# Kernel tuning notes

Hardware: AMD Instinct MI355X
Metric: run time of the kernel (lower is better)

## Reference

```python
import jax, jax.numpy as jnp
import numpy as np

N, D, IN_DIM, H, L = 20000, 32, 3, 64, 3


def _lstm_agg(h_nodes, nbr_sorted, W_ih, W_hh, b_ih, b_hh):
    """Batched LSTM over each node's (sorted) neighbor sequence; returns final hidden state h_T."""
    n = h_nodes.shape[0]
    hidden = W_hh.shape[1]

    def step(carry, idx):
        h, c = carry
        x = h_nodes[idx]                                     # [N, in_d] irregular gather
        gates = x @ W_ih.T + h @ W_hh.T + b_ih + b_hh        # [N, 4H], torch gate order i,f,g,o
        i_g, f_g, g_g, o_g = jnp.split(gates, 4, axis=-1)
        c = jax.nn.sigmoid(f_g) * c + jax.nn.sigmoid(i_g) * jnp.tanh(g_g)
        h = jax.nn.sigmoid(o_g) * jnp.tanh(c)
        return (h, c), None

    init = (jnp.zeros((n, hidden), h_nodes.dtype), jnp.zeros((n, hidden), h_nodes.dtype))
    (h_T, _), _ = jax.lax.scan(step, init, nbr_sorted.T)      # scan over D neighbor slots
    return h_T


def _layer(h, nbr_sorted, W_ih, W_hh, b_ih, b_hh, Wl, bl):
    agg = _lstm_agg(h, nbr_sorted, W_ih, W_hh, b_ih, b_hh)    # [N, H]
    comb = jnp.concatenate([h, agg], axis=-1)                 # [N, in_d + H]
    return jax.nn.relu(comb @ Wl.T + bl)


def _forward(node_features, nbr, params, W_out, b_out):
    nbr_sorted = jnp.sort(nbr, axis=1)   # permutation-invariant ordering (Eq. 9)
    h = node_features
    for p in params:
        h = _layer(h, nbr_sorted, *p)
    return (h @ W_out.T + b_out).squeeze(-1)   # [N] per-node log-likelihood scores


def setup_inputs():
    key = jax.random.key(0)
    ks = jax.random.split(key, 40)
    inp = {}
    inp["node_features"] = jax.random.normal(ks[0], (N, IN_DIM), jnp.float32)
    inp["nbr"] = jax.random.randint(ks[1], (N, D), 0, N, jnp.int32)
    k = 2
    s = 1.0 / np.sqrt(H)
    for l in range(L):
        in_d = IN_DIM if l == 0 else H
        inp[f"W_ih{l}"] = (jax.random.normal(ks[k], (4 * H, in_d)) * (1.0 / np.sqrt(in_d))).astype(jnp.float32); k += 1
        inp[f"W_hh{l}"] = (jax.random.normal(ks[k], (4 * H, H)) * s).astype(jnp.float32); k += 1
        inp[f"b_ih{l}"] = (jax.random.normal(ks[k], (4 * H,)) * s).astype(jnp.float32); k += 1
        inp[f"b_hh{l}"] = (jax.random.normal(ks[k], (4 * H,)) * s).astype(jnp.float32); k += 1
        inp[f"Wl{l}"] = (jax.random.normal(ks[k], (H, in_d + H)) * (1.0 / np.sqrt(in_d + H))).astype(jnp.float32); k += 1
        inp[f"bl{l}"] = (jax.random.normal(ks[k], (H,)) * s).astype(jnp.float32); k += 1
    inp["W_out"] = (jax.random.normal(ks[k], (1, H)) * s).astype(jnp.float32); k += 1
    inp["b_out"] = jnp.zeros((1,), jnp.float32)
    return inp


def reference(node_features, nbr, W_ih0, W_hh0, b_ih0, b_hh0, Wl0, bl0, W_ih1, W_hh1, b_ih1, b_hh1, Wl1, bl1, W_ih2, W_hh2, b_ih2, b_hh2, Wl2, bl2, W_out, b_out):
    params = [
        (W_ih0, W_hh0, b_ih0, b_hh0, Wl0, bl0),
        (W_ih1, W_hh1, b_ih1, b_hh1, Wl1, bl1),
        (W_ih2, W_hh2, b_ih2, b_hh2, Wl2, bl2),
    ]
    return _forward(node_features, nbr, params, W_out, b_out)
```

## Files before the change

### kernel.cpp

```cpp
#include <hip/hip_runtime.h>
#include <hip/hip_bf16.h>

#define NN 20000
#define NG 1250
#define LOG2E 1.44269504088896f
#define TWOLOG2E 2.88539008177793f

typedef __attribute__((ext_vector_type(8))) short short8;
typedef __attribute__((ext_vector_type(4))) float floatx4;

__device__ __forceinline__ floatx4 MF(short8 a, short8 b, floatx4 c) {
    return __builtin_amdgcn_mfma_f32_16x16x32_bf16(a, b, c, 0, 0, 0);
}
__device__ __forceinline__ float ex2(float x) { return __builtin_amdgcn_exp2f(x); }
__device__ __forceinline__ float rcp(float x) { return __builtin_amdgcn_rcpf(x); }
__device__ __forceinline__ unsigned short bf16r(float x) {
    return __builtin_bit_cast(unsigned short, __float2bfloat16(x));
}
__device__ __forceinline__ void lds_barrier() {
    asm volatile("s_waitcnt lgkmcnt(0)\n\ts_barrier" ::: "memory");
}
__device__ __forceinline__ int rowswz(int L) {
    return L ^ (((L >> 4) & 1) << 1) ^ ((L >> 3) & 1);
}

__global__ void sort_nbrs_kernel(const int* __restrict__ nbr, int* __restrict__ nbrT) {
    int n = blockIdx.x * blockDim.x + threadIdx.x;
    if (n >= NN) return;
    int v[32];
    const int4* src = (const int4*)(nbr + n * 32);
    #pragma unroll
    for (int i = 0; i < 8; i++) {
        int4 t = src[i];
        v[4*i] = t.x; v[4*i+1] = t.y; v[4*i+2] = t.z; v[4*i+3] = t.w;
    }
    #pragma unroll
    for (int k = 2; k <= 32; k <<= 1)
        #pragma unroll
        for (int j = k >> 1; j > 0; j >>= 1)
            #pragma unroll
            for (int i = 0; i < 32; i++) {
                int ixj = i ^ j;
                if (ixj > i) {
                    bool up = (i & k) == 0;
                    int a = v[i], b = v[ixj];
                    bool sw = up ? (a > b) : (a < b);
                    if (sw) { v[i] = b; v[ixj] = a; }
                }
            }
    int g = n >> 4, m = n & 15;
    int base = g * 512 + m;
    #pragma unroll
    for (int t = 0; t < 32; t++) nbrT[base + t * 16] = v[t];
}

#define PREP_TOT (49152 + 49152 + 12288 + 12288 + 768 + 640000)
__global__ void prep_kernel(const float* __restrict__ x,
    const float* __restrict__ Wih0, const float* __restrict__ Whh0,
    const float* __restrict__ bih0, const float* __restrict__ bhh0, const float* __restrict__ Wl0,
    const float* __restrict__ Wih1, const float* __restrict__ Whh1,
    const float* __restrict__ bih1, const float* __restrict__ bhh1, const float* __restrict__ Wl1,
    const float* __restrict__ Wih2, const float* __restrict__ Whh2,
    const float* __restrict__ bih2, const float* __restrict__ bhh2, const float* __restrict__ Wl2,
    unsigned short* __restrict__ Wih_p, unsigned short* __restrict__ Whh_p,
    unsigned short* __restrict__ Wlx_p, unsigned short* __restrict__ Wlh_p,
    float* __restrict__ bsum, unsigned short* __restrict__ x32)
{
    for (int i = blockIdx.x * 256 + threadIdx.x; i < PREP_TOT; i += gridDim.x * 256) {
        int j = i;
        if (j < 49152) {
            int l = j >> 14, e = j & 16383;
            if (l == 0) {
                if (e < 8192) {
                    int col = e >> 5, k = e & 31;
                    float sc = (col >= 128 && col < 192) ? TWOLOG2E : LOG2E;
                    float v = (k < 3) ? Wih0[col*3 + k] * sc : 0.f;
                    Wih_p[e] = bf16r(v);
                }
            } else {
                int col = e >> 6, k = e & 63;
                const float* W = (l == 1) ? Wih1 : Wih2;
                float sc = (col >= 128 && col < 192) ? TWOLOG2E : LOG2E;
                Wih_p[l*16384 + e] = bf16r(W[col*64 + k] * sc);
            }
            continue;
        }
        j -= 49152;
        if (j < 49152) {
            int l = j >> 14, e = j & 16383;
            int col = e >> 6, k = e & 63;
            const float* W = (l == 0) ? Whh0 : ((l == 1) ? Whh1 : Whh2);
            float sc = (col >= 128 && col < 192) ? TWOLOG2E : LOG2E;
            Whh_p[l*16384 + e] = bf16r(W[col*64 + k] * sc);
            continue;
        }
        j -= 49152;
        if (j < 12288) {
            int l = j >> 12, e = j & 4095;
            if (l == 0) {
                if (e < 2048) {
                    int col = e >> 5, k = e & 31;
                    float v = (k < 3) ? Wl0[col*67 + k] : 0.f;
                    Wlx_p[e] = bf16r(v);
                }
            } else {
                int col = e >> 6, k = e & 63;
                const float* W = (l == 1) ? Wl1 : Wl2;
                Wlx_p[l*4096 + e] = bf16r(W[col*128 + k]);
            }
            continue;
        }
        j -= 12288;
        if (j < 12288) {
            int l = j >> 12, e = j & 4095;
            int col = e >> 6, k = e & 63;
            float v = (l == 0) ? Wl0[col*67 + 3 + k]
                               : ((l == 1) ? Wl1 : Wl2)[col*128 + 64 + k];
            Wlh_p[l*4096 + e] = bf16r(v);
            continue;
        }
        j -= 12288;
        if (j < 768) {
            int l = j >> 8, col = j & 255;
            const float* bi = (l == 0) ? bih0 : ((l == 1) ? bih1 : bih2);
            const float* bh = (l == 0) ? bhh0 : ((l == 1) ? bhh1 : bhh2);
            float sc = (col >= 128 && col < 192) ? TWOLOG2E : LOG2E;
            bsum[l*256 + col] = (bi[col] + bh[col]) * sc;
            continue;
        }
        j -= 768;
        {
            int n = j >> 5, k = j & 31;
            x32[j] = bf16r((k < 3) ? x[n*3 + k] : 0.f);
        }
    }
}

template<int XKC, int LASTL>
__global__ __launch_bounds__(256, 3)
void lstm_mfma_kernel(const unsigned short* __restrict__ xsrc,
                      const int* __restrict__ nbrT,
                      const unsigned short* __restrict__ Wih,
                      const unsigned short* __restrict__ Whh,
                      const float* __restrict__ bsum,
                      const unsigned short* __restrict__ Wlx,
                      const unsigned short* __restrict__ Wlh,
                      const float* __restrict__ bl,
                      const float* __restrict__ W_out,
                      const float* __restrict__ b_out,
                      void* __restrict__ hout)
{
    __shared__ unsigned short sA[2][1024];
    __shared__ float sRed[64];

    const int w    = threadIdx.x >> 6;
    const int lane = threadIdx.x & 63;
    const int q    = lane >> 4;
    const int c    = lane & 15;
    const int XS   = XKC * 32;

    const int g = blockIdx.x;
    const int node0 = g * 16;
    const int* nbg = nbrT + g * 512;

    short8 fWih[4][XKC];
    short8 fWhh[4][2];
    float  biasv[4];
    #pragma unroll
    for (int t4 = 0; t4 < 4; t4++) {
        int col = 64*t4 + 16*w + c;
        biasv[t4] = bsum[col];
        #pragma unroll
        for (int kc = 0; kc < XKC; kc++)
            fWih[t4][kc] = *(const short8*)(Wih + col*XS + kc*32 + q*8);
        #pragma unroll
        for (int kc = 0; kc < 2; kc++)
            fWhh[t4][kc] = *(const short8*)(Whh + col*64 + kc*32 + q*8);
    }

    float cst[4] = {0.f, 0.f, 0.f, 0.f};
    short8 hA[2] = {};

    int idx_cur = nbg[c];
    int idx_nxt = nbg[16 + c];
    short8 xg[XKC];
    #pragma unroll
    for (int kc = 0; kc < XKC; kc++)
        xg[kc] = *(const short8*)(xsrc + (long)idx_cur * XS + kc*32 + q*8);

    #pragma unroll 1
    for (int t = 0; t < 32; t++) {
        floatx4 acc[4];
        #pragma unroll
        for (int t4 = 0; t4 < 4; t4++) {
            floatx4 a; a[0] = biasv[t4]; a[1] = biasv[t4]; a[2] = biasv[t4]; a[3] = biasv[t4];
            acc[t4] = a;
        }
        if (t > 0) {
            #pragma unroll
            for (int t4 = 0; t4 < 4; t4++) {
                acc[t4] = MF(hA[0], fWhh[t4][0], acc[t4]);
                acc[t4] = MF(hA[1], fWhh[t4][1], acc[t4]);
            }
        }
        #pragma unroll
        for (int t4 = 0; t4 < 4; t4++)
            #pragma unroll
            for (int kc = 0; kc < XKC; kc++)
                acc[t4] = MF(xg[kc], fWih[t4][kc], acc[t4]);

        if (t < 31) {
            #pragma unroll
            for (int kc = 0; kc < XKC; kc++)
                xg[kc] = *(const short8*)(xsrc + (long)idx_nxt * XS + kc*32 + q*8);
            int tn = (t + 2 < 32) ? t + 2 : 31;
            idx_nxt = nbg[tn*16 + c];
        }

        unsigned short* sAb = sA[t & 1];
        const int u = 16*w + c;
        #pragma unroll
        for (int r = 0; r < 4; r++) {
            float gi = acc[0][r], gf = acc[1][r], gg = acc[2][r], go = acc[3][r];
            float ei = ex2(-gi);
            float ef = ex2(-gf);
            float eo = ex2(-go);
            float eg = ex2(-__builtin_fabsf(gg));
            float iG = __builtin_copysignf(1.f - eg, gg) * rcp((1.f + ei) * (1.f + eg));
            float cm = fmaf(cst[r], rcp(1.f + ef), iG);
            cst[r] = cm;
            float ec = ex2(-TWOLOG2E * __builtin_fabsf(cm));
            float h  = __builtin_copysignf(1.f - ec, cm) * rcp((1.f + eo) * (1.f + ec));
            int row = (4*q + r) + 16*(u >> 3);
            sAb[rowswz(row)*8 + (u & 7)] = bf16r(h);
        }
        lds_barrier();
        hA[0] = *(const short8*)(sA[t & 1] + rowswz(lane)*8);
        hA[1] = *(const short8*)(sA[t & 1] + 512 + rowswz(lane)*8);
    }

    const int col = 16*w + c;
    short8 fx[XKC], fh[2];
    float blv = bl[col];
    #pragma unroll
    for (int kc = 0; kc < XKC; kc++)
        fx[kc] = *(const short8*)(Wlx + col*XS + kc*32 + q*8);
    fh[0] = *(const short8*)(Wlh + col*64 + q*8);
    fh[1] = *(const short8*)(Wlh + col*64 + 32 + q*8);
    short8 hin[XKC];
    #pragma unroll
    for (int kc = 0; kc < XKC; kc++)
        hin[kc] = *(const short8*)(xsrc + (long)(node0 + c) * XS + kc*32 + q*8);

    floatx4 a; a[0] = blv; a[1] = blv; a[2] = blv; a[3] = blv;
    #pragma unroll
    for (int kc = 0; kc < XKC; kc++) a = MF(hin[kc], fx[kc], a);
    a = MF(hA[0], fh[0], a);
    a = MF(hA[1], fh[1], a);

    if (!LASTL) {
        #pragma unroll
        for (int r = 0; r < 4; r++)
            ((unsigned short*)hout)[(node0 + 4*q + r) * 64 + col] = bf16r(fmaxf(a[r], 0.f));
    } else {
        float wo = W_out[col];
        float p[4];
        #pragma unroll
        for (int r = 0; r < 4; r++) p[r] = fmaxf(a[r], 0.f) * wo;
        #pragma unroll
        for (int d = 1; d < 16; d <<= 1) {
            #pragma unroll
            for (int r = 0; r < 4; r++) p[r] += __shfl_xor(p[r], d);
        }
        if (c == 0) {
            #pragma unroll
            for (int r = 0; r < 4; r++) sRed[w*16 + 4*q + r] = p[r];
        }
        lds_barrier();
        if (w == 0 && lane < 16)
            ((float*)hout)[node0 + lane] =
                sRed[lane] + sRed[16 + lane] + sRed[32 + lane] + sRed[48 + lane] + b_out[0];
    }
}

extern "C" void kernel_launch(void* const* d_in, const int* in_sizes, int n_in,
                              void* d_out, int out_size, void* d_ws, size_t ws_size,
                              hipStream_t stream) {
    (void)in_sizes; (void)n_in; (void)out_size; (void)ws_size;
    const float* node_features = (const float*)d_in[0];
    const int*   nbr           = (const int*)d_in[1];
    const float* Wih[3] = {(const float*)d_in[2],  (const float*)d_in[8],  (const float*)d_in[14]};
    const float* Whh[3] = {(const float*)d_in[3],  (const float*)d_in[9],  (const float*)d_in[15]};
    const float* bih[3] = {(const float*)d_in[4],  (const float*)d_in[10], (const float*)d_in[16]};
    const float* bhh[3] = {(const float*)d_in[5],  (const float*)d_in[11], (const float*)d_in[17]};
    const float* Wl[3]  = {(const float*)d_in[6],  (const float*)d_in[12], (const float*)d_in[18]};
    const float* bl[3]  = {(const float*)d_in[7],  (const float*)d_in[13], (const float*)d_in[19]};
    const float* W_out  = (const float*)d_in[20];
    const float* b_out  = (const float*)d_in[21];

    char* ws = (char*)d_ws;
    int*            nbrT  = (int*)ws;
    unsigned short* x32   = (unsigned short*)(ws + 2560000);
    unsigned short* hb1   = (unsigned short*)(ws + 3840000);
    unsigned short* hb2   = (unsigned short*)(ws + 6400000);
    unsigned short* Wih_p = (unsigned short*)(ws + 8960000);
    unsigned short* Whh_p = (unsigned short*)(ws + 9058304);
    unsigned short* Wlx_p = (unsigned short*)(ws + 9156608);
    unsigned short* Wlh_p = (unsigned short*)(ws + 9181184);
    float*          bsum  = (float*)(ws + 9205760);

    prep_kernel<<<1024, 256, 0, stream>>>(node_features,
        Wih[0], Whh[0], bih[0], bhh[0], Wl[0],
        Wih[1], Whh[1], bih[1], bhh[1], Wl[1],
        Wih[2], Whh[2], bih[2], bhh[2], Wl[2],
        Wih_p, Whh_p, Wlx_p, Wlh_p, bsum, x32);
    sort_nbrs_kernel<<<(NN + 255) / 256, 256, 0, stream>>>(nbr, nbrT);

    lstm_mfma_kernel<1, 0><<<NG, 256, 0, stream>>>(x32, nbrT,
        Wih_p,         Whh_p,         bsum,       Wlx_p,        Wlh_p,        bl[0],
        nullptr, nullptr, hb1);
    lstm_mfma_kernel<2, 0><<<NG, 256, 0, stream>>>(hb1, nbrT,
        Wih_p + 16384, Whh_p + 16384, bsum + 256, Wlx_p + 4096, Wlh_p + 4096, bl[1],
        nullptr, nullptr, hb2);
    lstm_mfma_kernel<2, 1><<<NG, 256, 0, stream>>>(hb2, nbrT,
        Wih_p + 32768, Whh_p + 32768, bsum + 512, Wlx_p + 8192, Wlh_p + 8192, bl[2],
        W_out, b_out, (float*)d_out);
}
```

Before: 297.1 us.

## Interleave two node groups per block and precompute input gates a step ahead

Each block now processes 32 nodes as two independent 16-node LSTM chains, interleaving their MFMAs and cell math so the serial recurrence latency of one chain is hidden by the other. The input-to-hidden MFMAs for the next step are issued right after the cell update, ahead of the barrier, and the gather prefetch runs one step further ahead. The second half of the W_ih fragments moves to LDS to save registers, and the neighbor sort is folded into the prep kernel to remove a launch. In exchange, register pressure is higher and the grid shrinks to 625 blocks, which lowers occupancy and wave-level parallelism.

```diff
diff --git a/kernel.cpp b/kernel.cpp
--- a/kernel.cpp
+++ b/kernel.cpp
@@ -2,7 +2,7 @@
 #include <hip/hip_bf16.h>
 
 #define NN 20000
-#define NG 1250
+#define NGB 625
 #define LOG2E 1.44269504088896f
 #define TWOLOG2E 2.88539008177793f
 
@@ -24,38 +24,27 @@
     return L ^ (((L >> 4) & 1) << 1) ^ ((L >> 3) & 1);
 }
 
-__global__ void sort_nbrs_kernel(const int* __restrict__ nbr, int* __restrict__ nbrT) {
-    int n = blockIdx.x * blockDim.x + threadIdx.x;
-    if (n >= NN) return;
-    int v[32];
-    const int4* src = (const int4*)(nbr + n * 32);
-    #pragma unroll
-    for (int i = 0; i < 8; i++) {
-        int4 t = src[i];
-        v[4*i] = t.x; v[4*i+1] = t.y; v[4*i+2] = t.z; v[4*i+3] = t.w;
-    }
-    #pragma unroll
-    for (int k = 2; k <= 32; k <<= 1)
-        #pragma unroll
-        for (int j = k >> 1; j > 0; j >>= 1)
-            #pragma unroll
-            for (int i = 0; i < 32; i++) {
-                int ixj = i ^ j;
-                if (ixj > i) {
-                    bool up = (i & k) == 0;
-                    int a = v[i], b = v[ixj];
-                    bool sw = up ? (a > b) : (a < b);
-                    if (sw) { v[i] = b; v[ixj] = a; }
-                }
-            }
-    int g = n >> 4, m = n & 15;
-    int base = g * 512 + m;
-    #pragma unroll
-    for (int t = 0; t < 32; t++) nbrT[base + t * 16] = v[t];
+__device__ __forceinline__ void lstm_cell4(const floatx4* acc, float* cst,
+                                           unsigned short* buf, int q, int u) {
+    #pragma unroll
+    for (int r = 0; r < 4; r++) {
+        float gi = acc[0][r], gf = acc[1][r], gg = acc[2][r], go = acc[3][r];
+        float ei = ex2(-gi);
+        float ef = ex2(-gf);
+        float eo = ex2(-go);
+        float eg = ex2(-__builtin_fabsf(gg));
+        float iG = __builtin_copysignf(1.f - eg, gg) * rcp((1.f + ei) * (1.f + eg));
+        float cm = fmaf(cst[r], rcp(1.f + ef), iG);
+        cst[r] = cm;
+        float ec = ex2(-TWOLOG2E * __builtin_fabsf(cm));
+        float h  = __builtin_copysignf(1.f - ec, cm) * rcp((1.f + eo) * (1.f + ec));
+        int row = 4*q + r + 16*(u >> 3);
+        buf[rowswz(row)*8 + (u & 7)] = bf16r(h);
+    }
 }
 
 #define PREP_TOT (49152 + 49152 + 12288 + 12288 + 768 + 640000)
-__global__ void prep_kernel(const float* __restrict__ x,
+__global__ void prep_kernel(const float* __restrict__ x, const int* __restrict__ nbr,
     const float* __restrict__ Wih0, const float* __restrict__ Whh0,
     const float* __restrict__ bih0, const float* __restrict__ bhh0, const float* __restrict__ Wl0,
     const float* __restrict__ Wih1, const float* __restrict__ Whh1,
@@ -64,8 +53,36 @@
     const float* __restrict__ bih2, const float* __restrict__ bhh2, const float* __restrict__ Wl2,
     unsigned short* __restrict__ Wih_p, unsigned short* __restrict__ Whh_p,
     unsigned short* __restrict__ Wlx_p, unsigned short* __restrict__ Wlh_p,
-    float* __restrict__ bsum, unsigned short* __restrict__ x32)
+    float* __restrict__ bsum, unsigned short* __restrict__ x32, int* __restrict__ nbrT)
 {
+    int tid = blockIdx.x * 256 + threadIdx.x;
+    if (tid < NN) {
+        int v[32];
+        const int4* src = (const int4*)(nbr + tid * 32);
+        #pragma unroll
+        for (int i = 0; i < 8; i++) {
+            int4 t = src[i];
+            v[4*i] = t.x; v[4*i+1] = t.y; v[4*i+2] = t.z; v[4*i+3] = t.w;
+        }
+        #pragma unroll
+        for (int k = 2; k <= 32; k <<= 1)
+            #pragma unroll
+            for (int j = k >> 1; j > 0; j >>= 1)
+                #pragma unroll
+                for (int i = 0; i < 32; i++) {
+                    int ixj = i ^ j;
+                    if (ixj > i) {
+                        bool up = (i & k) == 0;
+                        int a = v[i], b = v[ixj];
+                        bool sw = up ? (a > b) : (a < b);
+                        if (sw) { v[i] = b; v[ixj] = a; }
+                    }
+                }
+        int g = tid >> 5, m = tid & 31;
+        int base = g * 1024 + m;
+        #pragma unroll
+        for (int t = 0; t < 32; t++) nbrT[base + t * 32] = v[t];
+    }
     for (int i = blockIdx.x * 256 + threadIdx.x; i < PREP_TOT; i += gridDim.x * 256) {
         int j = i;
         if (j < 49152) {
@@ -150,8 +167,9 @@
                       const float* __restrict__ b_out,
                       void* __restrict__ hout)
 {
-    __shared__ unsigned short sA[2][1024];
-    __shared__ float sRed[64];
+    __shared__ unsigned short sWih[(XKC == 2) ? 256*36 : 16];
+    __shared__ unsigned short sA[2][2][1024];
+    __shared__ float sRed[2][4][16];
 
     const int w    = threadIdx.x >> 6;
     const int lane = threadIdx.x & 63;
@@ -160,126 +178,158 @@
     const int XS   = XKC * 32;
 
     const int g = blockIdx.x;
-    const int node0 = g * 16;
-    const int* nbg = nbrT + g * 512;
-
-    short8 fWih[4][XKC];
+    const int* nbg = nbrT + g * 1024;
+
+    if (XKC == 2) {
+        for (int i8 = threadIdx.x; i8 < 1024; i8 += 256) {
+            int col = i8 >> 2, ko = (i8 & 3) * 8;
+            *(short8*)(sWih + col*36 + ko) = *(const short8*)(Wih + col*64 + 32 + ko);
+        }
+    }
+
+    short8 fWih0[4];
     short8 fWhh[4][2];
     float  biasv[4];
     #pragma unroll
     for (int t4 = 0; t4 < 4; t4++) {
         int col = 64*t4 + 16*w + c;
-        biasv[t4] = bsum[col];
-        #pragma unroll
-        for (int kc = 0; kc < XKC; kc++)
-            fWih[t4][kc] = *(const short8*)(Wih + col*XS + kc*32 + q*8);
-        #pragma unroll
-        for (int kc = 0; kc < 2; kc++)
-            fWhh[t4][kc] = *(const short8*)(Whh + col*64 + kc*32 + q*8);
-    }
-
-    float cst[4] = {0.f, 0.f, 0.f, 0.f};
-    short8 hA[2] = {};
-
-    int idx_cur = nbg[c];
-    int idx_nxt = nbg[16 + c];
-    short8 xg[XKC];
-    #pragma unroll
-    for (int kc = 0; kc < XKC; kc++)
-        xg[kc] = *(const short8*)(xsrc + (long)idx_cur * XS + kc*32 + q*8);
+        biasv[t4]   = bsum[col];
+        fWih0[t4]   = *(const short8*)(Wih + col*XS + q*8);
+        fWhh[t4][0] = *(const short8*)(Whh + col*64 + q*8);
+        fWhh[t4][1] = *(const short8*)(Whh + col*64 + 32 + q*8);
+    }
+    __syncthreads();
+
+    int idxA = nbg[c], idxB = nbg[16 + c];
+    short8 xgA[XKC], xgB[XKC];
+    #pragma unroll
+    for (int kc = 0; kc < XKC; kc++) {
+        xgA[kc] = *(const short8*)(xsrc + (long)idxA * XS + kc*32 + q*8);
+        xgB[kc] = *(const short8*)(xsrc + (long)idxB * XS + kc*32 + q*8);
+    }
+    floatx4 accA[4], accB[4];
+    #pragma unroll
+    for (int t4 = 0; t4 < 4; t4++) {
+        floatx4 bb; bb[0] = biasv[t4]; bb[1] = biasv[t4]; bb[2] = biasv[t4]; bb[3] = biasv[t4];
+        accA[t4] = MF(xgA[0], fWih0[t4], bb);
+        accB[t4] = MF(xgB[0], fWih0[t4], bb);
+        if (XKC == 2) {
+            short8 wf = *(const short8*)(sWih + (64*t4 + 16*w + c)*36 + q*8);
+            accA[t4] = MF(xgA[1], wf, accA[t4]);
+            accB[t4] = MF(xgB[1], wf, accB[t4]);
+        }
+    }
+    idxA = nbg[32 + c]; idxB = nbg[48 + c];
+    #pragma unroll
+    for (int kc = 0; kc < XKC; kc++) {
+        xgA[kc] = *(const short8*)(xsrc + (long)idxA * XS + kc*32 + q*8);
+        xgB[kc] = *(const short8*)(xsrc + (long)idxB * XS + kc*32 + q*8);
+    }
+    int idxA2 = nbg[64 + c], idxB2 = nbg[80 + c];
+
+    float cstA[4] = {0.f,0.f,0.f,0.f}, cstB[4] = {0.f,0.f,0.f,0.f};
+    short8 hAA[2], hAB[2];
+    const int u = 16*w + c;
 
     #pragma unroll 1
     for (int t = 0; t < 32; t++) {
-        floatx4 acc[4];
-        #pragma unroll
-        for (int t4 = 0; t4 < 4; t4++) {
-            floatx4 a; a[0] = biasv[t4]; a[1] = biasv[t4]; a[2] = biasv[t4]; a[3] = biasv[t4];
-            acc[t4] = a;
-        }
         if (t > 0) {
             #pragma unroll
             for (int t4 = 0; t4 < 4; t4++) {
-                acc[t4] = MF(hA[0], fWhh[t4][0], acc[t4]);
-                acc[t4] = MF(hA[1], fWhh[t4][1], acc[t4]);
-            }
-        }
-        #pragma unroll
-        for (int t4 = 0; t4 < 4; t4++)
-            #pragma unroll
-            for (int kc = 0; kc < XKC; kc++)
-                acc[t4] = MF(xg[kc], fWih[t4][kc], acc[t4]);
+                accA[t4] = MF(hAA[0], fWhh[t4][0], accA[t4]);
+                accA[t4] = MF(hAA[1], fWhh[t4][1], accA[t4]);
+                accB[t4] = MF(hAB[0], fWhh[t4][0], accB[t4]);
+                accB[t4] = MF(hAB[1], fWhh[t4][1], accB[t4]);
+            }
+        }
+        unsigned short* bufA = sA[(t+1) & 1][0];
+        unsigned short* bufB = sA[(t+1) & 1][1];
+        lstm_cell4(accA, cstA, bufA, q, u);
+        lstm_cell4(accB, cstB, bufB, q, u);
 
         if (t < 31) {
             #pragma unroll
-            for (int kc = 0; kc < XKC; kc++)
-                xg[kc] = *(const short8*)(xsrc + (long)idx_nxt * XS + kc*32 + q*8);
-            int tn = (t + 2 < 32) ? t + 2 : 31;
-            idx_nxt = nbg[tn*16 + c];
-        }
-
-        unsigned short* sAb = sA[t & 1];
-        const int u = 16*w + c;
+            for (int t4 = 0; t4 < 4; t4++) {
+                floatx4 bb; bb[0] = biasv[t4]; bb[1] = biasv[t4]; bb[2] = biasv[t4]; bb[3] = biasv[t4];
+                accA[t4] = MF(xgA[0], fWih0[t4], bb);
+                accB[t4] = MF(xgB[0], fWih0[t4], bb);
+                if (XKC == 2) {
+                    short8 wf = *(const short8*)(sWih + (64*t4 + 16*w + c)*36 + q*8);
+                    accA[t4] = MF(xgA[1], wf, accA[t4]);
+                    accB[t4] = MF(xgB[1], wf, accB[t4]);
+                }
+            }
+            if (t < 30) {
+                #pragma unroll
+                for (int kc = 0; kc < XKC; kc++) {
+                    xgA[kc] = *(const short8*)(xsrc + (long)idxA2 * XS + kc*32 + q*8);
+                    xgB[kc] = *(const short8*)(xsrc + (long)idxB2 * XS + kc*32 + q*8);
+                }
+                int tn = (t + 3 < 32) ? t + 3 : 31;
+                idxA2 = nbg[tn*32 + c];
+                idxB2 = nbg[tn*32 + 16 + c];
+            }
+        }
+        lds_barrier();
+        const unsigned short* rdA = sA[(t+1) & 1][0];
+        const unsigned short* rdB = sA[(t+1) & 1][1];
+        hAA[0] = *(const short8*)(rdA + rowswz(lane)*8);
+        hAA[1] = *(const short8*)(rdA + 512 + rowswz(lane)*8);
+        hAB[0] = *(const short8*)(rdB + rowswz(lane)*8);
+        hAB[1] = *(const short8*)(rdB + 512 + rowswz(lane)*8);
+    }
+
+    const int col = 16*w + c;
+    short8 fx0 = *(const short8*)(Wlx + col*XS + q*8);
+    short8 fx1 = {};
+    if (XKC == 2) fx1 = *(const short8*)(Wlx + col*64 + 32 + q*8);
+    short8 fh0 = *(const short8*)(Wlh + col*64 + q*8);
+    short8 fh1 = *(const short8*)(Wlh + col*64 + 32 + q*8);
+    float blv = bl[col];
+
+    short8 hinA[XKC], hinB[XKC];
+    #pragma unroll
+    for (int kc = 0; kc < XKC; kc++) {
+        hinA[kc] = *(const short8*)(xsrc + (long)(32*g + c) * XS + kc*32 + q*8);
+        hinB[kc] = *(const short8*)(xsrc + (long)(32*g + 16 + c) * XS + kc*32 + q*8);
+    }
+    floatx4 aA, aB;
+    aA[0] = blv; aA[1] = blv; aA[2] = blv; aA[3] = blv;
+    aB = aA;
+    aA = MF(hinA[0], fx0, aA);
+    aB = MF(hinB[0], fx0, aB);
+    if (XKC == 2) { aA = MF(hinA[1], fx1, aA); aB = MF(hinB[1], fx1, aB); }
+    aA = MF(hAA[0], fh0, aA); aA = MF(hAA[1], fh1, aA);
+    aB = MF(hAB[0], fh0, aB); aB = MF(hAB[1], fh1, aB);
+
+    if (!LASTL) {
+        unsigned short* ho = (unsigned short*)hout;
         #pragma unroll
         for (int r = 0; r < 4; r++) {
-            float gi = acc[0][r], gf = acc[1][r], gg = acc[2][r], go = acc[3][r];
-            float ei = ex2(-gi);
-            float ef = ex2(-gf);
-            float eo = ex2(-go);
-            float eg = ex2(-__builtin_fabsf(gg));
-            float iG = __builtin_copysignf(1.f - eg, gg) * rcp((1.f + ei) * (1.f + eg));
-            float cm = fmaf(cst[r], rcp(1.f + ef), iG);
-            cst[r] = cm;
-            float ec = ex2(-TWOLOG2E * __builtin_fabsf(cm));
-            float h  = __builtin_copysignf(1.f - ec, cm) * rcp((1.f + eo) * (1.f + ec));
-            int row = (4*q + r) + 16*(u >> 3);
-            sAb[rowswz(row)*8 + (u & 7)] = bf16r(h);
-        }
-        lds_barrier();
-        hA[0] = *(const short8*)(sA[t & 1] + rowswz(lane)*8);
-        hA[1] = *(const short8*)(sA[t & 1] + 512 + rowswz(lane)*8);
-    }
-
-    const int col = 16*w + c;
-    short8 fx[XKC], fh[2];
-    float blv = bl[col];
-    #pragma unroll
-    for (int kc = 0; kc < XKC; kc++)
-        fx[kc] = *(const short8*)(Wlx + col*XS + kc*32 + q*8);
-    fh[0] = *(const short8*)(Wlh + col*64 + q*8);
-    fh[1] = *(const short8*)(Wlh + col*64 + 32 + q*8);
-    short8 hin[XKC];
-    #pragma unroll
-    for (int kc = 0; kc < XKC; kc++)
-        hin[kc] = *(const short8*)(xsrc + (long)(node0 + c) * XS + kc*32 + q*8);
-
-    floatx4 a; a[0] = blv; a[1] = blv; a[2] = blv; a[3] = blv;
-    #pragma unroll
-    for (int kc = 0; kc < XKC; kc++) a = MF(hin[kc], fx[kc], a);
-    a = MF(hA[0], fh[0], a);
-    a = MF(hA[1], fh[1], a);
-
-    if (!LASTL) {
-        #pragma unroll
-        for (int r = 0; r < 4; r++)
-            ((unsigned short*)hout)[(node0 + 4*q + r) * 64 + col] = bf16r(fmaxf(a[r], 0.f));
+            ho[(32*g + 4*q + r) * 64 + col]      = bf16r(fmaxf(aA[r], 0.f));
+            ho[(32*g + 16 + 4*q + r) * 64 + col] = bf16r(fmaxf(aB[r], 0.f));
+        }
     } else {
         float wo = W_out[col];
-        float p[4];
-        #pragma unroll
-        for (int r = 0; r < 4; r++) p[r] = fmaxf(a[r], 0.f) * wo;
+        float pA[4], pB[4];
+        #pragma unroll
+        for (int r = 0; r < 4; r++) { pA[r] = fmaxf(aA[r], 0.f) * wo; pB[r] = fmaxf(aB[r], 0.f) * wo; }
         #pragma unroll
         for (int d = 1; d < 16; d <<= 1) {
             #pragma unroll
-            for (int r = 0; r < 4; r++) p[r] += __shfl_xor(p[r], d);
+            for (int r = 0; r < 4; r++) { pA[r] += __shfl_xor(pA[r], d); pB[r] += __shfl_xor(pB[r], d); }
         }
         if (c == 0) {
             #pragma unroll
-            for (int r = 0; r < 4; r++) sRed[w*16 + 4*q + r] = p[r];
+            for (int r = 0; r < 4; r++) { sRed[0][w][4*q + r] = pA[r]; sRed[1][w][4*q + r] = pB[r]; }
         }
         lds_barrier();
-        if (w == 0 && lane < 16)
-            ((float*)hout)[node0 + lane] =
-                sRed[lane] + sRed[16 + lane] + sRed[32 + lane] + sRed[48 + lane] + b_out[0];
+        if (w == 0 && lane < 16) {
+            float* outf = (float*)hout;
+            float bo = b_out[0];
+            outf[32*g + lane]      = sRed[0][0][lane] + sRed[0][1][lane] + sRed[0][2][lane] + sRed[0][3][lane] + bo;
+            outf[32*g + 16 + lane] = sRed[1][0][lane] + sRed[1][1][lane] + sRed[1][2][lane] + sRed[1][3][lane] + bo;
+        }
     }
 }
 
@@ -309,20 +359,19 @@
     unsigned short* Wlh_p = (unsigned short*)(ws + 9181184);
     float*          bsum  = (float*)(ws + 9205760);
 
-    prep_kernel<<<1024, 256, 0, stream>>>(node_features,
+    prep_kernel<<<1024, 256, 0, stream>>>(node_features, nbr,
         Wih[0], Whh[0], bih[0], bhh[0], Wl[0],
         Wih[1], Whh[1], bih[1], bhh[1], Wl[1],
         Wih[2], Whh[2], bih[2], bhh[2], Wl[2],
-        Wih_p, Whh_p, Wlx_p, Wlh_p, bsum, x32);
-    sort_nbrs_kernel<<<(NN + 255) / 256, 256, 0, stream>>>(nbr, nbrT);
-
-    lstm_mfma_kernel<1, 0><<<NG, 256, 0, stream>>>(x32, nbrT,
+        Wih_p, Whh_p, Wlx_p, Wlh_p, bsum, x32, nbrT);
+
+    lstm_mfma_kernel<1, 0><<<NGB, 256, 0, stream>>>(x32, nbrT,
         Wih_p,         Whh_p,         bsum,       Wlx_p,        Wlh_p,        bl[0],
         nullptr, nullptr, hb1);
-    lstm_mfma_kernel<2, 0><<<NG, 256, 0, stream>>>(hb1, nbrT,
+    lstm_mfma_kernel<2, 0><<<NGB, 256, 0, stream>>>(hb1, nbrT,
         Wih_p + 16384, Whh_p + 16384, bsum + 256, Wlx_p + 4096, Wlh_p + 4096, bl[1],
         nullptr, nullptr, hb2);
-    lstm_mfma_kernel<2, 1><<<NG, 256, 0, stream>>>(hb2, nbrT,
+    lstm_mfma_kernel<2, 1><<<NGB, 256, 0, stream>>>(hb2, nbrT,
         Wih_p + 32768, Whh_p + 32768, bsum + 512, Wlx_p + 8192, Wlh_p + 8192, bl[2],
         W_out, b_out, (float*)d_out);
 }
```

After: 309.8 us. 1.04x slower.

## Software-pipeline input-gate MFMAs ahead of recurrence and fuse neighbor sort into prep

Applied to the files above, without the earlier changes.

The input-to-hidden MFMAs for the next timestep are now issued before the LDS barrier, so only the recurrent MFMAs stay on the serial critical path. The neighbor-gather prefetch is pushed two steps ahead. The gate math is rewritten with clamped exponents and a single reciprocal for the cell update to shorten the transcendental chain. The separate sort kernel is folded into the prep kernel, saving one launch. Clamping changes numerics slightly, and the extra live registers may reduce occupancy.

```diff
diff --git a/kernel.cpp b/kernel.cpp
--- a/kernel.cpp
+++ b/kernel.cpp
@@ -14,6 +14,9 @@
 }
 __device__ __forceinline__ float ex2(float x) { return __builtin_amdgcn_exp2f(x); }
 __device__ __forceinline__ float rcp(float x) { return __builtin_amdgcn_rcpf(x); }
+__device__ __forceinline__ float clamp30(float x) {
+    return __builtin_fminf(__builtin_fmaxf(x, -30.f), 30.f);
+}
 __device__ __forceinline__ unsigned short bf16r(float x) {
     return __builtin_bit_cast(unsigned short, __float2bfloat16(x));
 }
@@ -24,38 +27,29 @@
     return L ^ (((L >> 4) & 1) << 1) ^ ((L >> 3) & 1);
 }
 
-__global__ void sort_nbrs_kernel(const int* __restrict__ nbr, int* __restrict__ nbrT) {
-    int n = blockIdx.x * blockDim.x + threadIdx.x;
-    if (n >= NN) return;
-    int v[32];
-    const int4* src = (const int4*)(nbr + n * 32);
-    #pragma unroll
-    for (int i = 0; i < 8; i++) {
-        int4 t = src[i];
-        v[4*i] = t.x; v[4*i+1] = t.y; v[4*i+2] = t.z; v[4*i+3] = t.w;
-    }
-    #pragma unroll
-    for (int k = 2; k <= 32; k <<= 1)
-        #pragma unroll
-        for (int j = k >> 1; j > 0; j >>= 1)
-            #pragma unroll
-            for (int i = 0; i < 32; i++) {
-                int ixj = i ^ j;
-                if (ixj > i) {
-                    bool up = (i & k) == 0;
-                    int a = v[i], b = v[ixj];
-                    bool sw = up ? (a > b) : (a < b);
-                    if (sw) { v[i] = b; v[ixj] = a; }
-                }
-            }
-    int g = n >> 4, m = n & 15;
-    int base = g * 512 + m;
-    #pragma unroll
-    for (int t = 0; t < 32; t++) nbrT[base + t * 16] = v[t];
+__device__ __forceinline__ void lstm_cell4(const floatx4* acc, float* cst,
+                                           unsigned short* buf, int q, int u) {
+    #pragma unroll
+    for (int r = 0; r < 4; r++) {
+        float gi = clamp30(acc[0][r]);
+        float gf = clamp30(acc[1][r]);
+        float gg = clamp30(acc[2][r]);
+        float go = clamp30(acc[3][r]);
+        float ei = ex2(-gi), ef = ex2(-gf), eg = ex2(-gg), eo = ex2(-go);
+        float pf = 1.f + ef;
+        float p  = (1.f + ei) * (1.f + eg);
+        float num = fmaf(cst[r], p, (1.f - eg) * pf);
+        float cm  = num * rcp(p * pf);
+        cst[r] = cm;
+        float ec = ex2(-clamp30(TWOLOG2E * cm));
+        float h  = (1.f - ec) * rcp((1.f + eo) * (1.f + ec));
+        int row = 4*q + r + 16*(u >> 3);
+        buf[rowswz(row)*8 + (u & 7)] = bf16r(h);
+    }
 }
 
 #define PREP_TOT (49152 + 49152 + 12288 + 12288 + 768 + 640000)
-__global__ void prep_kernel(const float* __restrict__ x,
+__global__ void prep_kernel(const float* __restrict__ x, const int* __restrict__ nbr,
     const float* __restrict__ Wih0, const float* __restrict__ Whh0,
     const float* __restrict__ bih0, const float* __restrict__ bhh0, const float* __restrict__ Wl0,
     const float* __restrict__ Wih1, const float* __restrict__ Whh1,
@@ -64,8 +58,36 @@
     const float* __restrict__ bih2, const float* __restrict__ bhh2, const float* __restrict__ Wl2,
     unsigned short* __restrict__ Wih_p, unsigned short* __restrict__ Whh_p,
     unsigned short* __restrict__ Wlx_p, unsigned short* __restrict__ Wlh_p,
-    float* __restrict__ bsum, unsigned short* __restrict__ x32)
+    float* __restrict__ bsum, unsigned short* __restrict__ x32, int* __restrict__ nbrT)
 {
+    int tid = blockIdx.x * 256 + threadIdx.x;
+    if (tid < NN) {
+        int v[32];
+        const int4* src = (const int4*)(nbr + tid * 32);
+        #pragma unroll
+        for (int i = 0; i < 8; i++) {
+            int4 t = src[i];
+            v[4*i] = t.x; v[4*i+1] = t.y; v[4*i+2] = t.z; v[4*i+3] = t.w;
+        }
+        #pragma unroll
+        for (int k = 2; k <= 32; k <<= 1)
+            #pragma unroll
+            for (int j = k >> 1; j > 0; j >>= 1)
+                #pragma unroll
+                for (int i = 0; i < 32; i++) {
+                    int ixj = i ^ j;
+                    if (ixj > i) {
+                        bool up = (i & k) == 0;
+                        int a = v[i], b = v[ixj];
+                        bool sw = up ? (a > b) : (a < b);
+                        if (sw) { v[i] = b; v[ixj] = a; }
+                    }
+                }
+        int g = tid >> 4, m = tid & 15;
+        int base = g * 512 + m;
+        #pragma unroll
+        for (int t = 0; t < 32; t++) nbrT[base + t * 16] = v[t];
+    }
     for (int i = blockIdx.x * 256 + threadIdx.x; i < PREP_TOT; i += gridDim.x * 256) {
         int j = i;
         if (j < 49152) {
@@ -173,29 +195,35 @@
         #pragma unroll
         for (int kc = 0; kc < XKC; kc++)
             fWih[t4][kc] = *(const short8*)(Wih + col*XS + kc*32 + q*8);
-        #pragma unroll
-        for (int kc = 0; kc < 2; kc++)
-            fWhh[t4][kc] = *(const short8*)(Whh + col*64 + kc*32 + q*8);
-    }
+        fWhh[t4][0] = *(const short8*)(Whh + col*64 + q*8);
+        fWhh[t4][1] = *(const short8*)(Whh + col*64 + 32 + q*8);
+    }
+
+    int idx = nbg[c];
+    short8 xg[XKC];
+    #pragma unroll
+    for (int kc = 0; kc < XKC; kc++)
+        xg[kc] = *(const short8*)(xsrc + (long)idx * XS + kc*32 + q*8);
+
+    floatx4 acc[4];
+    #pragma unroll
+    for (int t4 = 0; t4 < 4; t4++) {
+        floatx4 bb; bb[0] = biasv[t4]; bb[1] = biasv[t4]; bb[2] = biasv[t4]; bb[3] = biasv[t4];
+        acc[t4] = MF(xg[0], fWih[t4][0], bb);
+        if (XKC == 2) acc[t4] = MF(xg[1], fWih[t4][1], acc[t4]);
+    }
+    idx = nbg[16 + c];
+    #pragma unroll
+    for (int kc = 0; kc < XKC; kc++)
+        xg[kc] = *(const short8*)(xsrc + (long)idx * XS + kc*32 + q*8);
+    int idx2 = nbg[32 + c];
 
     float cst[4] = {0.f, 0.f, 0.f, 0.f};
-    short8 hA[2] = {};
-
-    int idx_cur = nbg[c];
-    int idx_nxt = nbg[16 + c];
-    short8 xg[XKC];
-    #pragma unroll
-    for (int kc = 0; kc < XKC; kc++)
-        xg[kc] = *(const short8*)(xsrc + (long)idx_cur * XS + kc*32 + q*8);
+    short8 hA[2];
+    const int u = 16*w + c;
 
     #pragma unroll 1
     for (int t = 0; t < 32; t++) {
-        floatx4 acc[4];
-        #pragma unroll
-        for (int t4 = 0; t4 < 4; t4++) {
-            floatx4 a; a[0] = biasv[t4]; a[1] = biasv[t4]; a[2] = biasv[t4]; a[3] = biasv[t4];
-            acc[t4] = a;
-        }
         if (t > 0) {
             #pragma unroll
             for (int t4 = 0; t4 < 4; t4++) {
@@ -203,50 +231,38 @@
                 acc[t4] = MF(hA[1], fWhh[t4][1], acc[t4]);
             }
         }
-        #pragma unroll
-        for (int t4 = 0; t4 < 4; t4++)
-            #pragma unroll
-            for (int kc = 0; kc < XKC; kc++)
-                acc[t4] = MF(xg[kc], fWih[t4][kc], acc[t4]);
+        unsigned short* buf = sA[(t + 1) & 1];
+        lstm_cell4(acc, cst, buf, q, u);
 
         if (t < 31) {
             #pragma unroll
-            for (int kc = 0; kc < XKC; kc++)
-                xg[kc] = *(const short8*)(xsrc + (long)idx_nxt * XS + kc*32 + q*8);
-            int tn = (t + 2 < 32) ? t + 2 : 31;
-            idx_nxt = nbg[tn*16 + c];
-        }
-
-        unsigned short* sAb = sA[t & 1];
-        const int u = 16*w + c;
-        #pragma unroll
-        for (int r = 0; r < 4; r++) {
-            float gi = acc[0][r], gf = acc[1][r], gg = acc[2][r], go = acc[3][r];
-            float ei = ex2(-gi);
-            float ef = ex2(-gf);
-            float eo = ex2(-go);
-            float eg = ex2(-__builtin_fabsf(gg));
-            float iG = __builtin_copysignf(1.f - eg, gg) * rcp((1.f + ei) * (1.f + eg));
-            float cm = fmaf(cst[r], rcp(1.f + ef), iG);
-            cst[r] = cm;
-            float ec = ex2(-TWOLOG2E * __builtin_fabsf(cm));
-            float h  = __builtin_copysignf(1.f - ec, cm) * rcp((1.f + eo) * (1.f + ec));
-            int row = (4*q + r) + 16*(u >> 3);
-            sAb[rowswz(row)*8 + (u & 7)] = bf16r(h);
+            for (int t4 = 0; t4 < 4; t4++) {
+                floatx4 bb; bb[0] = biasv[t4]; bb[1] = biasv[t4]; bb[2] = biasv[t4]; bb[3] = biasv[t4];
+                acc[t4] = MF(xg[0], fWih[t4][0], bb);
+                if (XKC == 2) acc[t4] = MF(xg[1], fWih[t4][1], acc[t4]);
+            }
+            if (t < 30) {
+                #pragma unroll
+                for (int kc = 0; kc < XKC; kc++)
+                    xg[kc] = *(const short8*)(xsrc + (long)idx2 * XS + kc*32 + q*8);
+                int tn = (t + 3 < 32) ? t + 3 : 31;
+                idx2 = nbg[tn*16 + c];
+            }
         }
         lds_barrier();
-        hA[0] = *(const short8*)(sA[t & 1] + rowswz(lane)*8);
-        hA[1] = *(const short8*)(sA[t & 1] + 512 + rowswz(lane)*8);
+        const unsigned short* rd = sA[(t + 1) & 1];
+        hA[0] = *(const short8*)(rd + rowswz(lane)*8);
+        hA[1] = *(const short8*)(rd + 512 + rowswz(lane)*8);
     }
 
     const int col = 16*w + c;
-    short8 fx[XKC], fh[2];
+    short8 fx[XKC], fh0, fh1;
     float blv = bl[col];
     #pragma unroll
     for (int kc = 0; kc < XKC; kc++)
         fx[kc] = *(const short8*)(Wlx + col*XS + kc*32 + q*8);
-    fh[0] = *(const short8*)(Wlh + col*64 + q*8);
-    fh[1] = *(const short8*)(Wlh + col*64 + 32 + q*8);
+    fh0 = *(const short8*)(Wlh + col*64 + q*8);
+    fh1 = *(const short8*)(Wlh + col*64 + 32 + q*8);
     short8 hin[XKC];
     #pragma unroll
     for (int kc = 0; kc < XKC; kc++)
@@ -255,8 +271,8 @@
     floatx4 a; a[0] = blv; a[1] = blv; a[2] = blv; a[3] = blv;
     #pragma unroll
     for (int kc = 0; kc < XKC; kc++) a = MF(hin[kc], fx[kc], a);
-    a = MF(hA[0], fh[0], a);
-    a = MF(hA[1], fh[1], a);
+    a = MF(hA[0], fh0, a);
+    a = MF(hA[1], fh1, a);
 
     if (!LASTL) {
         #pragma unroll
@@ -309,12 +325,11 @@
     unsigned short* Wlh_p = (unsigned short*)(ws + 9181184);
     float*          bsum  = (float*)(ws + 9205760);
 
-    prep_kernel<<<1024, 256, 0, stream>>>(node_features,
+    prep_kernel<<<1024, 256, 0, stream>>>(node_features, nbr,
         Wih[0], Whh[0], bih[0], bhh[0], Wl[0],
         Wih[1], Whh[1], bih[1], bhh[1], Wl[1],
         Wih[2], Whh[2], bih[2], bhh[2], Wl[2],
-        Wih_p, Whh_p, Wlx_p, Wlh_p, bsum, x32);
-    sort_nbrs_kernel<<<(NN + 255) / 256, 256, 0, stream>>>(nbr, nbrT);
+        Wih_p, Whh_p, Wlx_p, Wlh_p, bsum, x32, nbrT);
 
     lstm_mfma_kernel<1, 0><<<NG, 256, 0, stream>>>(x32, nbrT,
         Wih_p,         Whh_p,         bsum,       Wlx_p,        Wlh_p,        bl[0],
```

After: 323.9 us. +9.0%, slower.
